# Kernel tuning notes

Measured on AMD Instinct MI355X. Metric: run time of the kernel, lower is better.

The kernel has to match this reference:

```python
import jax, jax.numpy as jnp
from jax import lax
import numpy as np

B, Q, H, D = 4, 128, 32, 128
L = 4096
END = 1024  # cache_index: tokens already in cache


def setup_inputs() -> dict:
    key = jax.random.key(0)
    k1, k2, k3, k4, k5 = jax.random.split(key, 5)
    query = jax.random.normal(k1, (B, Q, H, D), jnp.float32)
    k_new = jax.random.normal(k2, (B, Q, H, D), jnp.float32)
    v_new = jax.random.normal(k3, (B, Q, H, D), jnp.float32)
    cache_key = jax.random.normal(k4, (B, L, H, D), jnp.float32)
    cache_value = jax.random.normal(k5, (B, L, H, D), jnp.float32)
    attention_mask = jnp.ones((B, L), dtype=jnp.bool_)
    # standard lower-triangular causal mask over the full cache length
    causal_mask = jnp.tril(jnp.ones((L, L), dtype=jnp.bool_))[None, None, :, :]
    return {
        "query": query,
        "key": k_new,
        "value": v_new,
        "cache_key": cache_key,
        "cache_value": cache_value,
        "attention_mask": attention_mask,
        "causal_mask": causal_mask,
        "cache_index": END,
    }


def reference(query, key, value, cache_key, cache_value, attention_mask, causal_mask, cache_index):
    """Faithful port of FlaxAttentionModule._concatenate_to_cache (quantizer = identity)."""
    b, q, h, d = query.shape
    max_length = cache_key.shape[1]
    dtype = query.dtype

    # attention_mask [B, L] -> [B, 1, 1, L]
    am = attention_mask[:, None, None, :]

    # slice causal mask rows for the current update window: [1, 1, q, L]
    cm = lax.dynamic_slice(causal_mask, (0, 0, cache_index, 0), (1, 1, q, max_length))
    cm = jnp.broadcast_to(cm, (b,) + cm.shape[1:])
    am = jnp.logical_and(jnp.broadcast_to(am, cm.shape), cm)

    # in-place cache update at the rotated write position
    slice_indices = (0, cache_index % max_length, 0, 0)
    value_cache = lax.dynamic_update_slice(cache_value, value.astype(cache_value.dtype), slice_indices)
    key_cache = lax.dynamic_update_slice(cache_key, key.astype(cache_key.dtype), slice_indices)

    # mask out not-yet-written cache slots
    pad_mask = jnp.broadcast_to(
        jnp.arange(max_length) < cache_index + q, (b, 1, q, max_length)
    )
    am = jnp.logical_and(pad_mask, am)

    # init_attention_bias(): 0 where attended, dtype-min elsewhere
    bias = jnp.where(
        am,
        jnp.zeros((), dtype),
        jnp.full((), jnp.finfo(dtype).min, dtype),
    )
    return key_cache, value_cache, bias
```

## Files before the change

kernel.cpp:

```cpp
#include <hip/hip_runtime.h>

#define B_BATCH 4
#define Q_NEW   128
#define H_HEADS 32
#define D_HEAD  128
#define L_CACHE 4096

using mask_t = unsigned char;

__global__ __launch_bounds__(256) void cache_update_kernel(
    const float4* __restrict__ key_new,
    const float4* __restrict__ val_new,
    const float4* __restrict__ cache_key,
    const float4* __restrict__ cache_val,
    float4* __restrict__ out_key,
    float4* __restrict__ out_val,
    const int* __restrict__ cache_index_p)
{
    const long total = (long)B_BATCH * L_CACHE * (H_HEADS * D_HEAD / 4);
    int start = (*cache_index_p) % L_CACHE;
    if (start < 0) start = 0;
    if (start > L_CACHE - Q_NEW) start = L_CACHE - Q_NEW;

    const long stride = (long)gridDim.x * blockDim.x;
    for (long i = (long)blockIdx.x * blockDim.x + threadIdx.x; i < total; i += stride) {
        const long row = i >> 10;
        const int  l   = (int)(row & (L_CACHE - 1));
        const int  rel = l - start;
        float4 k, v;
        if ((unsigned)rel < (unsigned)Q_NEW) {
            const long b   = row >> 12;
            const long src = ((b * Q_NEW + rel) << 10) | (i & 1023);
            k = key_new[src];
            v = val_new[src];
        } else {
            k = cache_key[i];
            v = cache_val[i];
        }
        out_key[i] = k;
        out_val[i] = v;
    }
}

__global__ __launch_bounds__(256) void bias_kernel(
    const mask_t* __restrict__ att,
    const mask_t* __restrict__ causal,
    float4* __restrict__ bias_out,
    const int* __restrict__ cache_index_p)
{
    const long total = (long)B_BATCH * Q_NEW * (L_CACHE / 4);
    const long idx = (long)blockIdx.x * blockDim.x + threadIdx.x;
    if (idx >= total) return;

    const int ci = *cache_index_p;
    int crow = ci;
    if (crow < 0) crow = 0;
    if (crow > L_CACHE - Q_NEW) crow = L_CACHE - Q_NEW;

    const int  j4   = (int)(idx & (L_CACHE / 4 - 1));
    const long rowi = idx >> 10;
    const int  i    = (int)(rowi & (Q_NEW - 1));
    const int  b    = (int)(rowi >> 7);

    const uchar4 a4 = *(const uchar4*)(att + (long)b * L_CACHE + j4 * 4);
    const uchar4 c4 = *(const uchar4*)(causal + (long)(crow + i) * L_CACHE + j4 * 4);

    const int   jb        = j4 * 4;
    const int   pad_limit = ci + Q_NEW;
    const float NEG       = __int_as_float(0xFF7F7FFF);

    float4 o;
    o.x = (a4.x && c4.x && (jb + 0) < pad_limit) ? 0.0f : NEG;
    o.y = (a4.y && c4.y && (jb + 1) < pad_limit) ? 0.0f : NEG;
    o.z = (a4.z && c4.z && (jb + 2) < pad_limit) ? 0.0f : NEG;
    o.w = (a4.w && c4.w && (jb + 3) < pad_limit) ? 0.0f : NEG;
    bias_out[idx] = o;
}

extern "C" void kernel_launch(void* const* d_in, const int* in_sizes, int n_in,
                              void* d_out, int out_size, void* d_ws, size_t ws_size,
                              hipStream_t stream) {
    const float4* key_new   = (const float4*)d_in[1];
    const float4* val_new   = (const float4*)d_in[2];
    const float4* cache_key = (const float4*)d_in[3];
    const float4* cache_val = (const float4*)d_in[4];
    const mask_t* att       = (const mask_t*)d_in[5];
    const mask_t* causal    = (const mask_t*)d_in[6];
    const int*    cache_idx = (const int*)d_in[7];

    float* out = (float*)d_out;
    const long cache_elems = (long)B_BATCH * L_CACHE * H_HEADS * D_HEAD;
    float4* out_key  = (float4*)(out);
    float4* out_val  = (float4*)(out + cache_elems);
    float4* bias_out = (float4*)(out + 2 * cache_elems);

    cache_update_kernel<<<2048, 256, 0, stream>>>(
        key_new, val_new, cache_key, cache_val, out_key, out_val, cache_idx);

    bias_kernel<<<2048, 256, 0, stream>>>(att, causal, bias_out, cache_idx);
}
```

Before: 226.0 us.

## Fuse cache copy and bias kernels with nontemporal loads and stores

```diff
diff --git a/kernel.cpp b/kernel.cpp
--- a/kernel.cpp
+++ b/kernel.cpp
@@ -6,96 +6,96 @@
 #define D_HEAD  128
 #define L_CACHE 4096
 
+#define NTHREADS 524288
+#define CACHE_F4 16777216
+#define ITERS    32
+
+typedef float f4 __attribute__((ext_vector_type(4)));
 using mask_t = unsigned char;
 
-__global__ __launch_bounds__(256) void cache_update_kernel(
-    const float4* __restrict__ key_new,
-    const float4* __restrict__ val_new,
-    const float4* __restrict__ cache_key,
-    const float4* __restrict__ cache_val,
-    float4* __restrict__ out_key,
-    float4* __restrict__ out_val,
+__global__ __launch_bounds__(256) void fused_cache_bias_kernel(
+    const f4* __restrict__ key_new,
+    const f4* __restrict__ val_new,
+    const f4* __restrict__ cache_key,
+    const f4* __restrict__ cache_val,
+    f4* __restrict__ out_key,
+    f4* __restrict__ out_val,
+    const mask_t* __restrict__ att,
+    const mask_t* __restrict__ causal,
+    f4* __restrict__ bias_out,
     const int* __restrict__ cache_index_p)
 {
-    const long total = (long)B_BATCH * L_CACHE * (H_HEADS * D_HEAD / 4);
-    int start = (*cache_index_p) % L_CACHE;
+    const int tid = blockIdx.x * 256 + threadIdx.x;
+    const int ci  = *cache_index_p;
+
+    int start = ci % L_CACHE;
     if (start < 0) start = 0;
     if (start > L_CACHE - Q_NEW) start = L_CACHE - Q_NEW;
 
-    const long stride = (long)gridDim.x * blockDim.x;
-    for (long i = (long)blockIdx.x * blockDim.x + threadIdx.x; i < total; i += stride) {
-        const long row = i >> 10;
-        const int  l   = (int)(row & (L_CACHE - 1));
-        const int  rel = l - start;
-        float4 k, v;
+    {
+        int crow = ci;
+        if (crow < 0) crow = 0;
+        if (crow > L_CACHE - Q_NEW) crow = L_CACHE - Q_NEW;
+
+        const int j4   = tid & (L_CACHE / 4 - 1);
+        const int rowi = tid >> 10;
+        const int qi   = rowi & (Q_NEW - 1);
+        const int b    = rowi >> 7;
+
+        const uchar4 a4 = *(const uchar4*)(att + b * L_CACHE + j4 * 4);
+        const uchar4 c4 = *(const uchar4*)(causal + (long)(crow + qi) * L_CACHE + j4 * 4);
+
+        const int jb        = j4 * 4;
+        const int pad_limit = ci + Q_NEW;
+        const float NEG = __int_as_float(0xFF7F7FFF);
+
+        f4 o;
+        o.x = (a4.x && c4.x && (jb + 0) < pad_limit) ? 0.0f : NEG;
+        o.y = (a4.y && c4.y && (jb + 1) < pad_limit) ? 0.0f : NEG;
+        o.z = (a4.z && c4.z && (jb + 2) < pad_limit) ? 0.0f : NEG;
+        o.w = (a4.w && c4.w && (jb + 3) < pad_limit) ? 0.0f : NEG;
+        __builtin_nontemporal_store(o, &bias_out[tid]);
+    }
+
+#pragma unroll 8
+    for (int t = 0; t < ITERS; ++t) {
+        const int i   = tid + t * NTHREADS;
+        const int row = i >> 10;
+        const int l   = row & (L_CACHE - 1);
+        const int rel = l - start;
+        f4 k, v;
         if ((unsigned)rel < (unsigned)Q_NEW) {
-            const long b   = row >> 12;
-            const long src = ((b * Q_NEW + rel) << 10) | (i & 1023);
-            k = key_new[src];
-            v = val_new[src];
+            const int b   = row >> 12;
+            const int src = ((b * Q_NEW + rel) << 10) | (i & 1023);
+            k = __builtin_nontemporal_load(&key_new[src]);
+            v = __builtin_nontemporal_load(&val_new[src]);
         } else {
-            k = cache_key[i];
-            v = cache_val[i];
+            k = __builtin_nontemporal_load(&cache_key[i]);
+            v = __builtin_nontemporal_load(&cache_val[i]);
         }
-        out_key[i] = k;
-        out_val[i] = v;
+        __builtin_nontemporal_store(k, &out_key[i]);
+        __builtin_nontemporal_store(v, &out_val[i]);
     }
-}
-
-__global__ __launch_bounds__(256) void bias_kernel(
-    const mask_t* __restrict__ att,
-    const mask_t* __restrict__ causal,
-    float4* __restrict__ bias_out,
-    const int* __restrict__ cache_index_p)
-{
-    const long total = (long)B_BATCH * Q_NEW * (L_CACHE / 4);
-    const long idx = (long)blockIdx.x * blockDim.x + threadIdx.x;
-    if (idx >= total) return;
-
-    const int ci = *cache_index_p;
-    int crow = ci;
-    if (crow < 0) crow = 0;
-    if (crow > L_CACHE - Q_NEW) crow = L_CACHE - Q_NEW;
-
-    const int  j4   = (int)(idx & (L_CACHE / 4 - 1));
-    const long rowi = idx >> 10;
-    const int  i    = (int)(rowi & (Q_NEW - 1));
-    const int  b    = (int)(rowi >> 7);
-
-    const uchar4 a4 = *(const uchar4*)(att + (long)b * L_CACHE + j4 * 4);
-    const uchar4 c4 = *(const uchar4*)(causal + (long)(crow + i) * L_CACHE + j4 * 4);
-
-    const int   jb        = j4 * 4;
-    const int   pad_limit = ci + Q_NEW;
-    const float NEG       = __int_as_float(0xFF7F7FFF);
-
-    float4 o;
-    o.x = (a4.x && c4.x && (jb + 0) < pad_limit) ? 0.0f : NEG;
-    o.y = (a4.y && c4.y && (jb + 1) < pad_limit) ? 0.0f : NEG;
-    o.z = (a4.z && c4.z && (jb + 2) < pad_limit) ? 0.0f : NEG;
-    o.w = (a4.w && c4.w && (jb + 3) < pad_limit) ? 0.0f : NEG;
-    bias_out[idx] = o;
 }
 
 extern "C" void kernel_launch(void* const* d_in, const int* in_sizes, int n_in,
                               void* d_out, int out_size, void* d_ws, size_t ws_size,
                               hipStream_t stream) {
-    const float4* key_new   = (const float4*)d_in[1];
-    const float4* val_new   = (const float4*)d_in[2];
-    const float4* cache_key = (const float4*)d_in[3];
-    const float4* cache_val = (const float4*)d_in[4];
+    const f4*     key_new   = (const f4*)d_in[1];
+    const f4*     val_new   = (const f4*)d_in[2];
+    const f4*     cache_key = (const f4*)d_in[3];
+    const f4*     cache_val = (const f4*)d_in[4];
     const mask_t* att       = (const mask_t*)d_in[5];
     const mask_t* causal    = (const mask_t*)d_in[6];
     const int*    cache_idx = (const int*)d_in[7];
 
     float* out = (float*)d_out;
     const long cache_elems = (long)B_BATCH * L_CACHE * H_HEADS * D_HEAD;
-    float4* out_key  = (float4*)(out);
-    float4* out_val  = (float4*)(out + cache_elems);
-    float4* bias_out = (float4*)(out + 2 * cache_elems);
+    f4* out_key  = (f4*)(out);
+    f4* out_val  = (f4*)(out + cache_elems);
+    f4* bias_out = (f4*)(out + 2 * cache_elems);
 
-    cache_update_kernel<<<2048, 256, 0, stream>>>(
-        key_new, val_new, cache_key, cache_val, out_key, out_val, cache_idx);
-
-    bias_kernel<<<2048, 256, 0, stream>>>(att, causal, bias_out, cache_idx);
+    fused_cache_bias_kernel<<<2048, 256, 0, stream>>>(
+        key_new, val_new, cache_key, cache_val, out_key, out_val,
+        att, causal, bias_out, cache_idx);
 }
```

New measurement: 202.7 us. 10.3% less time.
